# Optimization experiments

Measured on AMD Instinct MI355X. Metric: run time of the kernel, lower is better.

The kernel has to match this reference:

```python
import jax, jax.numpy as jnp
import numpy as np

NBATCH, NATOM, NEIGH = 16, 512, 64
NTYPE, NWAVE, NIPSIN, NORBIT = 4, 8, 3, 128
CUTOFF = 5.0
NPAIR = NATOM * NEIGH  # neighbor pairs per configuration


def _make_index_para(nipsin):
    # [0, 1,1,1, 2,...(9 times)] -> angular-order label per channel
    parts = [np.zeros(1, np.int32)]
    for i in range(1, nipsin):
        parts.append(np.full(3 ** i, i, np.int32))
    return jnp.asarray(np.concatenate(parts))


def setup_inputs() -> dict:
    key = jax.random.key(0)
    ks = jax.random.split(key, 10)
    cart = jax.random.uniform(ks[0], (NBATCH, NATOM, 3), jnp.float32) * 6.0
    numatoms = jnp.full((NBATCH,), NATOM, dtype=jnp.int32)
    species = jax.random.randint(ks[1], (NBATCH * NATOM,), 0, NTYPE).astype(jnp.int32)
    atom_index = jax.random.randint(ks[2], (2, NBATCH, NPAIR), 0, NATOM).astype(jnp.int32)
    shifts = jnp.zeros((NBATCH, NPAIR, 3), jnp.float32)  # all pairs valid (pass >-1e10 check)
    # learned parameters / buffers
    rs = jnp.tile(jnp.linspace(0.5, 4.0, NWAVE, dtype=jnp.float32)[None, :], (NTYPE, 1))
    inta = -(jax.random.uniform(ks[3], (NTYPE, NWAVE), jnp.float32) * 0.9 + 0.1)
    params = jnp.ones((NTYPE, NWAVE), jnp.float32) / float(NEIGH)
    hyper = jax.random.normal(ks[4], (1, NIPSIN, NWAVE, NORBIT), jnp.float32) * (1.0 / np.sqrt(NWAVE))
    index_para = _make_index_para(NIPSIN)
    return {"cart": cart, "numatoms": numatoms, "species": species,
            "atom_index": atom_index, "shifts": shifts,
            "rs": rs, "inta": inta, "params": params, "hyper": hyper,
            "index_para": index_para, "cutoff": CUTOFF}


def _angular(dist_vec, f_cut, nipsin):
    # dist_vec: [N,3], f_cut: [N] -> [L, N] with L = 1 + 3 + ... + 3^(nipsin-1)
    dv = dist_vec.T  # [3, N]
    orb = f_cut[None, :]
    parts = [orb]
    for _ in range(1, nipsin):
        orb = (orb[:, None, :] * dv[None, :, :]).reshape(-1, dv.shape[1])
        parts.append(orb)
    return jnp.concatenate(parts, axis=0)


def reference(cart, numatoms, species, atom_index, shifts, rs, inta, params, hyper, index_para, cutoff):
    nbatch, natom, _ = cart.shape
    totnatom = nbatch * natom
    cart_ = cart.reshape(totnatom, 3)
    # offset per-config neighbor indices to global atom ids
    offs = (jnp.arange(nbatch, dtype=atom_index.dtype) * natom)[None, :, None]
    idx12 = (atom_index + offs).reshape(2, -1)  # [2, Npairs]
    dist_vec = cart_[idx12[0]] - cart_[idx12[1]] + shifts.reshape(-1, 3)  # [Npairs,3]
    distances = jnp.linalg.norm(dist_vec, axis=-1)  # [Npairs]
    sp_j = species[idx12[1]]
    f_cut = jnp.square(0.5 * jnp.cos(distances * (jnp.pi / cutoff)) + 0.5)
    # per-pair gaussian radial basis, gathered by neighbor element type
    radial = jnp.exp(inta[sp_j] * jnp.square(distances[:, None] - rs[sp_j]))  # [Npairs, nwave]
    ang = _angular(dist_vec, f_cut, NIPSIN)  # [L, Npairs]
    orbital = ang.T[:, :, None] * radial[:, None, :]  # [Npairs, L, nwave]
    orb_coeff = params[species]  # [totnatom, nwave] (all species >= 0)
    # iteration 0 (ocmod_list is empty, so no refinement loop)
    worb = orbital * orb_coeff[idx12[1]][:, None, :]  # [Npairs, L, nwave]
    sum_worb = jax.ops.segment_sum(worb, idx12[0], num_segments=totnatom)  # [totnatom, L, nwave]
    hp = hyper[0][index_para]  # [L, nwave, norbit]
    hw = jnp.einsum('ijk,jkm->ijm', sum_worb, hp)  # [totnatom, L, norbit]
    density = jnp.sum(jnp.square(hw), axis=1)  # [totnatom, norbit]
    return density
```

## Files before the change

kernel.cpp:

```cpp
#include <hip/hip_runtime.h>
#include <hip/hip_bf16.h>

#define NBATCH  16
#define NATOM   512
#define NEIGH   64
#define NPAIR   (NATOM * NEIGH)
#define TOTPAIR (NBATCH * NPAIR)
#define TOTATOM (NBATCH * NATOM)
#define NTYPE   4
#define NWAVE   8
#define NL      13
#define NORBIT  128
#define CAP     128
#define NSUB    8
#define SUBCAP  40
#define PAIRS_PER_SUB (NPAIR / NSUB)

#define AST     136
#define S2ST    40

#define WS_HFRAG_OFF 5505024

typedef __attribute__((ext_vector_type(8))) short  short8;
typedef __attribute__((ext_vector_type(4))) float  f32x4;

static __device__ inline unsigned short f2bf(float f) {
    unsigned u = __builtin_bit_cast(unsigned, f);
    u += 0x7FFFu + ((u >> 16) & 1u);
    return (unsigned short)(u >> 16);
}
static __device__ inline float bf2f(unsigned short h) {
    unsigned u = ((unsigned)h) << 16;
    return __builtin_bit_cast(float, u);
}

__global__ void hfrag_kernel(const float* __restrict__ hyper,
                             unsigned short* __restrict__ hfrag) {
    const int s    = blockIdx.x >> 3;
    const int n    = blockIdx.x & 7;
    const int lane = threadIdx.x;
    const int q    = lane >> 4;
    const int col  = n * 16 + (lane & 15);
#pragma unroll
    for (int j = 0; j < 8; ++j) {
        int k = q * 8 + j;
        float f = (k < 24) ? hyper[(k >> 3) * (NWAVE * NORBIT) + (k & 7) * NORBIT + col]
                           : 0.0f;
        unsigned short hi = f2bf(f);
        unsigned short v  = (s == 0) ? hi : f2bf(f - bf2f(hi));
        hfrag[((size_t)(blockIdx.x * 64 + lane)) * 8 + j] = v;
    }
}

__global__ __launch_bounds__(512) void fill_kernel(
    const int* __restrict__ atom_index,
    int*       __restrict__ count,
    unsigned short* __restrict__ bucket)
{
    const int b   = blockIdx.x >> 3;
    const int s   = blockIdx.x & 7;
    const int tid = threadIdx.x;

    __shared__ int s_cnt[NATOM];
    s_cnt[tid] = 0;
    __syncthreads();

#pragma unroll
    for (int it = 0; it < PAIRS_PER_SUB / 512; ++it) {
        int pl = s * PAIRS_PER_SUB + it * 512 + tid;
        int il = atom_index[b * NPAIR + pl];
        int slot = atomicAdd(&s_cnt[il], 1);
        if (slot < SUBCAP)
            bucket[((size_t)((b * NATOM + il) * NSUB + s)) * SUBCAP + slot] =
                (unsigned short)pl;
    }
    __syncthreads();

    count[(b * NATOM + tid) * NSUB + s] = s_cnt[tid];
}

__global__ __launch_bounds__(128) void gather_kernel(
    const float* __restrict__ cart,
    const int*   __restrict__ species,
    const int*   __restrict__ atom_index,
    const float* __restrict__ shifts,
    const float* __restrict__ rs,
    const float* __restrict__ inta,
    const float* __restrict__ params,
    const float* __restrict__ cutoff_p,
    const int*   __restrict__ count,
    const unsigned short* __restrict__ bucket,
    const unsigned short* __restrict__ hfrag,
    float*       __restrict__ out)
{
    const int i      = blockIdx.x;
    const int b      = i >> 9;
    const int base   = b << 9;
    const int tid    = threadIdx.x;
    const int lane   = tid & 63;
    const int waveId = tid >> 6;

    __shared__ __attribute__((aligned(16))) unsigned short s_A[16 * AST];
    __shared__ __attribute__((aligned(16))) unsigned short s_B[24 * AST];
    __shared__ __attribute__((aligned(16))) unsigned short s_S2[16 * S2ST];
    __shared__ float s_tab[3 * NTYPE * NWAVE];
    __shared__ int   s_cv[NSUB];
    __shared__ int   s_off[NSUB + 1];

    short8 hb[4], lb[4];
#pragma unroll
    for (int t = 0; t < 4; ++t) {
        int n = waveId * 4 + t;
        hb[t] = *(const short8*)&hfrag[((size_t)(n * 64 + lane)) * 8];
        lb[t] = *(const short8*)&hfrag[((size_t)((8 + n) * 64 + lane)) * 8];
    }

    if (tid < NTYPE * NWAVE) {
        s_tab[tid]                     = rs[tid];
        s_tab[NTYPE * NWAVE + tid]     = inta[tid];
        s_tab[2 * NTYPE * NWAVE + tid] = params[tid];
    }
    if (tid >= 64 && tid < 64 + NSUB) {
        int c = count[i * NSUB + (tid - 64)];
        s_cv[tid - 64] = c < SUBCAP ? c : SUBCAP;
    }
    for (int e = tid; e < 16 * S2ST; e += 128) s_S2[e] = 0;
    __syncthreads();

    if (tid == 0) {
        int o = 0;
#pragma unroll
        for (int s2 = 0; s2 < NSUB; ++s2) { s_off[s2] = o; o += s_cv[s2]; }
        s_off[NSUB] = o;
    }
    __syncthreads();

    int total = s_off[NSUB];
    if (total > CAP) total = CAP;
    const int T = (total + 31) >> 5;

    const float cx  = cart[3 * i + 0];
    const float cy  = cart[3 * i + 1];
    const float cz  = cart[3 * i + 2];
    const float pic = 3.14159265358979323846f / cutoff_p[0];

    if (tid < total) {
        const int k = tid;
        int s2 = 0;
#pragma unroll
        for (int t = 1; t < NSUB; ++t)
            if (k >= s_off[t]) s2 = t;
        int pl = (int)bucket[((size_t)(i * NSUB + s2)) * SUBCAP + (k - s_off[s2])];
        int p  = (b << 15) | pl;
        int j  = atom_index[TOTPAIR + p] + base;

        float dx = cx - cart[3 * j + 0] + shifts[3 * p + 0];
        float dy = cy - cart[3 * j + 1] + shifts[3 * p + 1];
        float dz = cz - cart[3 * j + 2] + shifts[3 * p + 2];
        float d  = sqrtf(dx * dx + dy * dy + dz * dz);

        float c  = 0.5f * __cosf(d * pic) + 0.5f;
        float fc = c * c;

        float a1 = fc * dx, a2 = fc * dy, a3 = fc * dz;
        s_A[0 * AST + k]  = f2bf(fc);
        s_A[1 * AST + k]  = f2bf(a1);      s_A[2 * AST + k]  = f2bf(a2);
        s_A[3 * AST + k]  = f2bf(a3);
        s_A[4 * AST + k]  = f2bf(a1 * dx); s_A[5 * AST + k]  = f2bf(a1 * dy);
        s_A[6 * AST + k]  = f2bf(a1 * dz);
        s_A[7 * AST + k]  = f2bf(a2 * dx); s_A[8 * AST + k]  = f2bf(a2 * dy);
        s_A[9 * AST + k]  = f2bf(a2 * dz);
        s_A[10 * AST + k] = f2bf(a3 * dx); s_A[11 * AST + k] = f2bf(a3 * dy);
        s_A[12 * AST + k] = f2bf(a3 * dz);

        int sp = species[j];
#pragma unroll
        for (int w = 0; w < NWAVE; ++w) {
            float tt = d - s_tab[sp * NWAVE + w];
            float rp = __expf(s_tab[NTYPE * NWAVE + sp * NWAVE + w] * tt * tt)
                     * s_tab[2 * NTYPE * NWAVE + sp * NWAVE + w];
            unsigned short hi = f2bf(rp);
            s_B[w * AST + k]       = hi;
            s_B[(8 + w) * AST + k] = f2bf(rp - bf2f(hi));
        }
    }
    if (T > 0 && total < T * 32) {
        int tb = (T - 1) << 5;
        for (int e = tid; e < 16 * 32; e += 128) {
            int row = e >> 5, k = tb + (e & 31);
            if (k >= total) { s_A[row * AST + k] = 0; s_B[row * AST + k] = 0; }
        }
    }
    __syncthreads();

    if (waveId == 0) {
        const int m = lane & 15, q = lane >> 4;
        f32x4 acc = {0.f, 0.f, 0.f, 0.f};
        for (int t = 0; t < T; ++t) {
            short8 af  = *(const short8*)&s_A[m * AST + t * 32 + q * 8];
            short8 bhf = *(const short8*)&s_B[m * AST + t * 32 + q * 8];
            short8 blf = *(const short8*)&s_B[(m + 8) * AST + t * 32 + q * 8];
            acc = __builtin_amdgcn_mfma_f32_16x16x32_bf16(af, bhf, acc, 0, 0, 0);
            acc = __builtin_amdgcn_mfma_f32_16x16x32_bf16(af, blf, acc, 0, 0, 0);
        }
        if (m < 8) {
#pragma unroll
            for (int reg = 0; reg < 4; ++reg) {
                int l = q * 4 + reg;
                if (l < 13) {
                    int ip = (l == 0) ? 0 : ((l < 4) ? 1 : 2);
                    s_S2[l * S2ST + ip * 8 + m] = f2bf(acc[reg]);
                }
            }
        }
    }
    __syncthreads();

    {
        const int m = lane & 15, q = lane >> 4;
        short8 sf = *(const short8*)&s_S2[m * S2ST + q * 8];
#pragma unroll
        for (int t = 0; t < 4; ++t) {
            f32x4 acc = {0.f, 0.f, 0.f, 0.f};
            acc = __builtin_amdgcn_mfma_f32_16x16x32_bf16(sf, hb[t], acc, 0, 0, 0);
            acc = __builtin_amdgcn_mfma_f32_16x16x32_bf16(sf, lb[t], acc, 0, 0, 0);
            float part = 0.f;
#pragma unroll
            for (int reg = 0; reg < 4; ++reg) {
                int l = q * 4 + reg;
                if (l < 13) part += acc[reg] * acc[reg];
            }
            part += __shfl_xor(part, 16);
            part += __shfl_xor(part, 32);
            if (lane < 16)
                out[(size_t)i * NORBIT + (waveId * 4 + t) * 16 + lane] = part;
        }
    }
}

extern "C" void kernel_launch(void* const* d_in, const int* in_sizes, int n_in,
                              void* d_out, int out_size, void* d_ws, size_t ws_size,
                              hipStream_t stream) {
    const float* cart       = (const float*)d_in[0];
    const int*   species    = (const int*)  d_in[2];
    const int*   atom_index = (const int*)  d_in[3];
    const float* shifts     = (const float*)d_in[4];
    const float* rs         = (const float*)d_in[5];
    const float* inta       = (const float*)d_in[6];
    const float* params     = (const float*)d_in[7];
    const float* hyper      = (const float*)d_in[8];
    const float* cutoff_p   = (const float*)d_in[10];

    int* count = (int*)d_ws;
    unsigned short* bucket =
        (unsigned short*)((char*)d_ws + (size_t)TOTATOM * NSUB * sizeof(int));
    unsigned short* hfrag = (unsigned short*)((char*)d_ws + WS_HFRAG_OFF);
    float* out = (float*)d_out;

    hfrag_kernel<<<16, 64, 0, stream>>>(hyper, hfrag);

    fill_kernel<<<NBATCH * NSUB, 512, 0, stream>>>(atom_index, count, bucket);

    gather_kernel<<<TOTATOM, 128, 0, stream>>>(
        cart, species, atom_index, shifts, rs, inta, params, cutoff_p,
        count, bucket, hfrag, out);
}
```

Measured before the change: 111.5 us.

## Compute per-pair features in fill kernel and bucket payloads for gather

Moves the per-pair geometry, cutoff, angular and radial basis computation from the per-atom gather kernel into the bucketing fill kernel, which now writes a 64-byte bf16 payload per pair instead of a pair index. The hyper fragment preparation is folded into the fill kernel, removing one launch, and the count layout is transposed. The gather kernel then only loads contiguous payload records, avoiding dependent index, cart and species lookups. The trade-off is much more workspace traffic (about 2M pairs x 64B written and read) and the fill kernel running only 128 blocks with heavier per-thread work.

After: 114.6 us. 1.03x slower.

```diff
diff --git a/kernel.cpp b/kernel.cpp
--- a/kernel.cpp
+++ b/kernel.cpp
@@ -19,7 +19,10 @@
 #define AST     136
 #define S2ST    40
 
-#define WS_HFRAG_OFF 5505024
+#define WS_COUNT_OFF 0
+#define WS_HFRAG_OFF 262144
+#define WS_PAY_OFF   278528
+
 
 typedef __attribute__((ext_vector_type(8))) short  short8;
 typedef __attribute__((ext_vector_type(4))) float  f32x4;
@@ -34,52 +37,7 @@
     return __builtin_bit_cast(float, u);
 }
 
-__global__ void hfrag_kernel(const float* __restrict__ hyper,
-                             unsigned short* __restrict__ hfrag) {
-    const int s    = blockIdx.x >> 3;
-    const int n    = blockIdx.x & 7;
-    const int lane = threadIdx.x;
-    const int q    = lane >> 4;
-    const int col  = n * 16 + (lane & 15);
-#pragma unroll
-    for (int j = 0; j < 8; ++j) {
-        int k = q * 8 + j;
-        float f = (k < 24) ? hyper[(k >> 3) * (NWAVE * NORBIT) + (k & 7) * NORBIT + col]
-                           : 0.0f;
-        unsigned short hi = f2bf(f);
-        unsigned short v  = (s == 0) ? hi : f2bf(f - bf2f(hi));
-        hfrag[((size_t)(blockIdx.x * 64 + lane)) * 8 + j] = v;
-    }
-}
-
 __global__ __launch_bounds__(512) void fill_kernel(
-    const int* __restrict__ atom_index,
-    int*       __restrict__ count,
-    unsigned short* __restrict__ bucket)
-{
-    const int b   = blockIdx.x >> 3;
-    const int s   = blockIdx.x & 7;
-    const int tid = threadIdx.x;
-
-    __shared__ int s_cnt[NATOM];
-    s_cnt[tid] = 0;
-    __syncthreads();
-
-#pragma unroll
-    for (int it = 0; it < PAIRS_PER_SUB / 512; ++it) {
-        int pl = s * PAIRS_PER_SUB + it * 512 + tid;
-        int il = atom_index[b * NPAIR + pl];
-        int slot = atomicAdd(&s_cnt[il], 1);
-        if (slot < SUBCAP)
-            bucket[((size_t)((b * NATOM + il) * NSUB + s)) * SUBCAP + slot] =
-                (unsigned short)pl;
-    }
-    __syncthreads();
-
-    count[(b * NATOM + tid) * NSUB + s] = s_cnt[tid];
-}
-
-__global__ __launch_bounds__(128) void gather_kernel(
     const float* __restrict__ cart,
     const int*   __restrict__ species,
     const int*   __restrict__ atom_index,
@@ -88,24 +46,111 @@
     const float* __restrict__ inta,
     const float* __restrict__ params,
     const float* __restrict__ cutoff_p,
-    const int*   __restrict__ count,
-    const unsigned short* __restrict__ bucket,
+    const float* __restrict__ hyper,
+    int*            __restrict__ count,
+    unsigned short* __restrict__ hfrag,
+    unsigned short* __restrict__ payload)
+{
+    const int bid = blockIdx.x;
+    const int b   = bid >> 3;
+    const int s   = bid & 7;
+    const int tid = threadIdx.x;
+
+    __shared__ int   s_cnt[NATOM];
+    __shared__ float s_tab[3 * NTYPE * NWAVE];
+
+    if (tid < NTYPE * NWAVE) {
+        s_tab[tid]                     = rs[tid];
+        s_tab[NTYPE * NWAVE + tid]     = inta[tid];
+        s_tab[2 * NTYPE * NWAVE + tid] = params[tid];
+    }
+    s_cnt[tid] = 0;
+
+    if (bid < 16 && tid < 64) {
+        const int hs = bid >> 3, n = bid & 7, lane = tid;
+        const int q = lane >> 4, col = n * 16 + (lane & 15);
+#pragma unroll
+        for (int j = 0; j < 8; ++j) {
+            int k = q * 8 + j;
+            float f = (k < 24)
+                ? hyper[(k >> 3) * (NWAVE * NORBIT) + (k & 7) * NORBIT + col]
+                : 0.0f;
+            unsigned short hi = f2bf(f);
+            unsigned short v  = hs ? f2bf(f - bf2f(hi)) : hi;
+            hfrag[((size_t)(bid * 64 + lane)) * 8 + j] = v;
+        }
+    }
+    __syncthreads();
+
+    const float pic = 3.14159265358979323846f / cutoff_p[0];
+    const int pbase = b * NPAIR;
+
+    for (int it = 0; it < PAIRS_PER_SUB / 512; ++it) {
+        int pl = s * PAIRS_PER_SUB + it * 512 + tid;
+        int p  = pbase + pl;
+        int il = atom_index[p];
+        int j  = atom_index[TOTPAIR + p] + (b << 9);
+        int i  = il + (b << 9);
+
+        float dx = cart[3 * i + 0] - cart[3 * j + 0] + shifts[3 * p + 0];
+        float dy = cart[3 * i + 1] - cart[3 * j + 1] + shifts[3 * p + 1];
+        float dz = cart[3 * i + 2] - cart[3 * j + 2] + shifts[3 * p + 2];
+        float d  = sqrtf(dx * dx + dy * dy + dz * dz);
+
+        float c  = 0.5f * __cosf(d * pic) + 0.5f;
+        float fc = c * c;
+
+        int slot = atomicAdd(&s_cnt[il], 1);
+        if (slot < SUBCAP) {
+            float a1 = fc * dx, a2 = fc * dy, a3 = fc * dz;
+            short8 v0, v1, v2, v3;
+            v0[0] = (short)f2bf(fc);
+            v0[1] = (short)f2bf(a1);      v0[2] = (short)f2bf(a2);
+            v0[3] = (short)f2bf(a3);
+            v0[4] = (short)f2bf(a1 * dx); v0[5] = (short)f2bf(a1 * dy);
+            v0[6] = (short)f2bf(a1 * dz); v0[7] = (short)f2bf(a2 * dx);
+            v1[0] = (short)f2bf(a2 * dy); v1[1] = (short)f2bf(a2 * dz);
+            v1[2] = (short)f2bf(a3 * dx); v1[3] = (short)f2bf(a3 * dy);
+            v1[4] = (short)f2bf(a3 * dz);
+            v1[5] = 0; v1[6] = 0; v1[7] = 0;
+
+            int sp = species[j];
+#pragma unroll
+            for (int w = 0; w < NWAVE; ++w) {
+                float tt = d - s_tab[sp * NWAVE + w];
+                float rp = __expf(s_tab[NTYPE * NWAVE + sp * NWAVE + w] * tt * tt)
+                         * s_tab[2 * NTYPE * NWAVE + sp * NWAVE + w];
+                unsigned short hi = f2bf(rp);
+                v2[w] = (short)hi;
+                v3[w] = (short)f2bf(rp - bf2f(hi));
+            }
+
+            short8* dst = (short8*)(payload +
+                (((size_t)((b * NATOM + il) * NSUB + s)) * SUBCAP + slot) * 32);
+            dst[0] = v0; dst[1] = v1; dst[2] = v2; dst[3] = v3;
+        }
+    }
+    __syncthreads();
+
+    count[s * TOTATOM + (b * NATOM + tid)] = s_cnt[tid];
+}
+
+__global__ __launch_bounds__(128) void gather_kernel(
+    const int*            __restrict__ count,
+    const unsigned short* __restrict__ payload,
     const unsigned short* __restrict__ hfrag,
-    float*       __restrict__ out)
+    float*                __restrict__ out)
 {
     const int i      = blockIdx.x;
-    const int b      = i >> 9;
-    const int base   = b << 9;
     const int tid    = threadIdx.x;
     const int lane   = tid & 63;
     const int waveId = tid >> 6;
 
     __shared__ __attribute__((aligned(16))) unsigned short s_A[16 * AST];
-    __shared__ __attribute__((aligned(16))) unsigned short s_B[24 * AST];
+    __shared__ __attribute__((aligned(16))) unsigned short s_B[16 * AST];
     __shared__ __attribute__((aligned(16))) unsigned short s_S2[16 * S2ST];
-    __shared__ float s_tab[3 * NTYPE * NWAVE];
-    __shared__ int   s_cv[NSUB];
-    __shared__ int   s_off[NSUB + 1];
+    __shared__ int s_cv[NSUB];
+    __shared__ int s_off[NSUB + 1];
 
     short8 hb[4], lb[4];
 #pragma unroll
@@ -115,14 +160,9 @@
         lb[t] = *(const short8*)&hfrag[((size_t)((8 + n) * 64 + lane)) * 8];
     }
 
-    if (tid < NTYPE * NWAVE) {
-        s_tab[tid]                     = rs[tid];
-        s_tab[NTYPE * NWAVE + tid]     = inta[tid];
-        s_tab[2 * NTYPE * NWAVE + tid] = params[tid];
-    }
-    if (tid >= 64 && tid < 64 + NSUB) {
-        int c = count[i * NSUB + (tid - 64)];
-        s_cv[tid - 64] = c < SUBCAP ? c : SUBCAP;
+    if (tid < NSUB) {
+        int c = count[tid * TOTATOM + i];
+        s_cv[tid] = c < SUBCAP ? c : SUBCAP;
     }
     for (int e = tid; e < 16 * S2ST; e += 128) s_S2[e] = 0;
     __syncthreads();
@@ -139,49 +179,33 @@
     if (total > CAP) total = CAP;
     const int T = (total + 31) >> 5;
 
-    const float cx  = cart[3 * i + 0];
-    const float cy  = cart[3 * i + 1];
-    const float cz  = cart[3 * i + 2];
-    const float pic = 3.14159265358979323846f / cutoff_p[0];
-
     if (tid < total) {
         const int k = tid;
         int s2 = 0;
 #pragma unroll
         for (int t = 1; t < NSUB; ++t)
             if (k >= s_off[t]) s2 = t;
-        int pl = (int)bucket[((size_t)(i * NSUB + s2)) * SUBCAP + (k - s_off[s2])];
-        int p  = (b << 15) | pl;
-        int j  = atom_index[TOTPAIR + p] + base;
-
-        float dx = cx - cart[3 * j + 0] + shifts[3 * p + 0];
-        float dy = cy - cart[3 * j + 1] + shifts[3 * p + 1];
-        float dz = cz - cart[3 * j + 2] + shifts[3 * p + 2];
-        float d  = sqrtf(dx * dx + dy * dy + dz * dz);
-
-        float c  = 0.5f * __cosf(d * pic) + 0.5f;
-        float fc = c * c;
-
-        float a1 = fc * dx, a2 = fc * dy, a3 = fc * dz;
-        s_A[0 * AST + k]  = f2bf(fc);
-        s_A[1 * AST + k]  = f2bf(a1);      s_A[2 * AST + k]  = f2bf(a2);
-        s_A[3 * AST + k]  = f2bf(a3);
-        s_A[4 * AST + k]  = f2bf(a1 * dx); s_A[5 * AST + k]  = f2bf(a1 * dy);
-        s_A[6 * AST + k]  = f2bf(a1 * dz);
-        s_A[7 * AST + k]  = f2bf(a2 * dx); s_A[8 * AST + k]  = f2bf(a2 * dy);
-        s_A[9 * AST + k]  = f2bf(a2 * dz);
-        s_A[10 * AST + k] = f2bf(a3 * dx); s_A[11 * AST + k] = f2bf(a3 * dy);
-        s_A[12 * AST + k] = f2bf(a3 * dz);
-
-        int sp = species[j];
+        const short8* rec = (const short8*)(payload +
+            (((size_t)(i * NSUB + s2)) * SUBCAP + (k - s_off[s2])) * 32);
+        short8 v0 = rec[0], v1 = rec[1], v2 = rec[2], v3 = rec[3];
+
+        s_A[0 * AST + k]  = (unsigned short)v0[0];
+        s_A[1 * AST + k]  = (unsigned short)v0[1];
+        s_A[2 * AST + k]  = (unsigned short)v0[2];
+        s_A[3 * AST + k]  = (unsigned short)v0[3];
+        s_A[4 * AST + k]  = (unsigned short)v0[4];
+        s_A[5 * AST + k]  = (unsigned short)v0[5];
+        s_A[6 * AST + k]  = (unsigned short)v0[6];
+        s_A[7 * AST + k]  = (unsigned short)v0[7];
+        s_A[8 * AST + k]  = (unsigned short)v1[0];
+        s_A[9 * AST + k]  = (unsigned short)v1[1];
+        s_A[10 * AST + k] = (unsigned short)v1[2];
+        s_A[11 * AST + k] = (unsigned short)v1[3];
+        s_A[12 * AST + k] = (unsigned short)v1[4];
 #pragma unroll
         for (int w = 0; w < NWAVE; ++w) {
-            float tt = d - s_tab[sp * NWAVE + w];
-            float rp = __expf(s_tab[NTYPE * NWAVE + sp * NWAVE + w] * tt * tt)
-                     * s_tab[2 * NTYPE * NWAVE + sp * NWAVE + w];
-            unsigned short hi = f2bf(rp);
-            s_B[w * AST + k]       = hi;
-            s_B[(8 + w) * AST + k] = f2bf(rp - bf2f(hi));
+            s_B[w * AST + k]       = (unsigned short)v2[w];
+            s_B[(8 + w) * AST + k] = (unsigned short)v3[w];
         }
     }
     if (T > 0 && total < T * 32) {
@@ -251,17 +275,14 @@
     const float* hyper      = (const float*)d_in[8];
     const float* cutoff_p   = (const float*)d_in[10];
 
-    int* count = (int*)d_ws;
-    unsigned short* bucket =
-        (unsigned short*)((char*)d_ws + (size_t)TOTATOM * NSUB * sizeof(int));
-    unsigned short* hfrag = (unsigned short*)((char*)d_ws + WS_HFRAG_OFF);
+    int*            count   = (int*)((char*)d_ws + WS_COUNT_OFF);
+    unsigned short* hfrag   = (unsigned short*)((char*)d_ws + WS_HFRAG_OFF);
+    unsigned short* payload = (unsigned short*)((char*)d_ws + WS_PAY_OFF);
     float* out = (float*)d_out;
 
-    hfrag_kernel<<<16, 64, 0, stream>>>(hyper, hfrag);
-
-    fill_kernel<<<NBATCH * NSUB, 512, 0, stream>>>(atom_index, count, bucket);
-
-    gather_kernel<<<TOTATOM, 128, 0, stream>>>(
-        cart, species, atom_index, shifts, rs, inta, params, cutoff_p,
-        count, bucket, hfrag, out);
-}
+    fill_kernel<<<NBATCH * NSUB, 512, 0, stream>>>(
+        cart, species, atom_index, shifts, rs, inta, params, cutoff_p, hyper,
+        count, hfrag, payload);
+
+    gather_kernel<<<TOTATOM, 128, 0, stream>>>(count, payload, hfrag, out);
+}
```
